# Performance work log

Measured on AMD Instinct MI355X. Metric: run time of the kernel, lower is better.

## Reference

```python
import jax, jax.numpy as jnp
import numpy as np

IGNORE_ID = -1
NEG_INF = -jnp.inf


def ctc_force_align(log_probs, ctc_label):
    """Viterbi forced alignment, vectorized over batch, scan over time.

    log_probs: [B, T, V] log-softmaxed CTC outputs (blank = 0).
    ctc_label: [B, L] int labels in [1, V).
    Returns align: [B, L] float32, begin frame (1-based, t+1) of each label.
    Assumes uniform lengths: input_len = T, target_len = L for every item
    (how the inputs are generated here).
    """
    B, T, V = log_probs.shape
    L = ctc_label.shape[1]
    N = 2 * L + 1  # CTC state lattice: blank,label,blank,...

    labels = jnp.zeros((B, N), dtype=ctc_label.dtype).at[:, 1::2].set(ctc_label)
    # per-state emission log-prob: [B, T, N]
    lab_b = jnp.broadcast_to(labels[:, None, :], (B, T, N))
    lp_states = jnp.take_along_axis(log_probs, lab_b, axis=2)

    idx = jnp.arange(N)
    ihalf = idx.astype(jnp.float32) / 2.0
    # labels[i] == labels[i-2] (False for i < 2)
    same_label = labels == jnp.concatenate(
        [jnp.full((B, 2), -1, labels.dtype), labels[:, :-2]], axis=1)
    two_way = (idx % 2 == 0)[None, :] | (idx == 1)[None, :] | same_label  # [B, N]

    ts = jnp.arange(T).astype(jnp.float32)
    # infeasible if i/2 > t or L - i/2 > T - t  (float division as in original)
    feas = ~((ihalf[None, :] > ts[:, None]) |
             (float(L) - ihalf[None, :] > float(T) - ts[:, None]))  # [T, N]

    a0 = jnp.where(idx[None, :] < 2, lp_states[:, 0, :], NEG_INF)  # [B, N]

    def shift(x, k):
        return jnp.pad(x, ((0, 0), (k, 0)), constant_values=NEG_INF)[:, :N]

    def step(a_prev, inputs):
        lp_t, feas_t = inputs  # [B, N], [N]
        p0, p1, p2 = a_prev, shift(a_prev, 1), shift(a_prev, 2)
        val_two = jnp.where(p0 > p1, idx, idx - 1)
        best0 = (p0 > p1) & (p0 > p2)
        best1 = (p1 > p0) & (p1 > p2)
        val_three = jnp.where(best0, idx, jnp.where(best1, idx - 1, idx - 2))
        val = jnp.where(idx[None, :] == 0, 0,
                        jnp.where(two_way, val_two, val_three))
        off = idx[None, :] - val
        a_sel = jnp.where(off == 0, p0, jnp.where(off == 1, p1, p2))
        a_new = jnp.where(feas_t[None, :], a_sel + lp_t, NEG_INF)
        v = jnp.where(feas_t[None, :], val, 0).astype(jnp.int32)
        return a_new, v

    lp_tb = jnp.moveaxis(lp_states, 1, 0)  # [T, B, N]
    a_final, v_all = jax.lax.scan(step, a0, (lp_tb[1:], feas[1:]))
    # v_all: [T-1, B, N] for t = 1 .. T-1
    v_all = jnp.moveaxis(v_all, 1, 0)  # [B, T-1, N]

    def backtrace(a_fin, v_seq):  # a_fin: [N], v_seq: [T-1, N]
        use_last = a_fin[N - 1] > a_fin[N - 2]
        pre0 = jnp.where(use_last, N - 1, N - 2)
        align0 = jnp.where((jnp.arange(L) == L - 1) & (~use_last),
                           float(T), 0.0).astype(jnp.float32)
        tp1 = jnp.arange(T - 1, 0, -1)  # t+1 values: T-1 .. 1
        lidx = jnp.arange(L)

        def bstep(carry, inp):
            pre, align = carry
            v_row, t1 = inp
            pre = v_row[pre]
            odd = (pre % 2) == 1
            align = jnp.where((lidx == pre // 2) & odd,
                              t1.astype(jnp.float32), align)
            return (pre, align), None

        (_, align), _ = jax.lax.scan(bstep, (pre0, align0), (v_seq[::-1], tp1))
        return align

    return jax.vmap(backtrace)(a_final, v_all)  # [B, L]


def setup_inputs() -> dict:
    key = jax.random.key(0)
    k0, k1, k2, k3, k4 = jax.random.split(key, 5)
    B, layers, L, T, V = 16, 6, 200, 1000, 5000
    ali_out = jax.random.uniform(k0, (B, layers, L + 1, T), dtype=jnp.float32)
    ali_beg = jax.random.randint(k1, (B, L), 0, T, dtype=jnp.int32)
    ali_end = jax.random.randint(k2, (B, L), 0, T, dtype=jnp.int32)
    enc_mask = jnp.zeros((B, T), dtype=bool)
    ctc_out = jax.random.normal(k3, (B, T, V), dtype=jnp.float32)
    ctc_label = jax.random.randint(k4, (B, L), 1, V, dtype=jnp.int32)
    ctc_len = jnp.full((B,), T, dtype=jnp.int32)
    return {"ali_out": ali_out, "ali_beg": ali_beg, "ali_end": ali_end,
            "enc_mask": enc_mask, "ctc_out": ctc_out,
            "ctc_label": ctc_label, "ctc_len": ctc_len}


def reference(ali_out, ali_beg, ali_end, enc_mask, ctc_out, ctc_label, ctc_len):
    B, layers, olen, ilen = ali_out.shape
    hlen = enc_mask.shape[1]  # == ilen == T
    # forced alignment on detached (stop-gradient) log-probs
    log_probs = jax.lax.stop_gradient(jax.nn.log_softmax(ctc_out, axis=2))
    ali = ctc_force_align(log_probs, ctc_label)  # [B, L] float32
    # expected position: matmul with pos_vec = [1..hlen], drop last output step
    pos = jnp.arange(1, hlen + 1, dtype=ali_out.dtype)
    ali_pos = jnp.einsum('bloi,i->blo', ali_out, pos)[:, :, :-1]  # [B, layers, L]
    ylens = jnp.sum(ali_beg != IGNORE_ID, axis=1)  # [B]
    mask = jnp.arange(olen - 1)[None, :] >= ylens[:, None]  # [B, L] pad mask
    total = (~mask).sum().astype(ali_out.dtype) * layers
    lat = jnp.where(mask[:, None, :], 0.0, ali_pos - ali[:, None, :])
    return (lat ** 2).sum() / total / hlen
```

## Files before the change

### kernel.cpp

```cpp
#include <hip/hip_runtime.h>
#include <hip/hip_bf16.h>
#include <math.h>

#define NEGINF (-INFINITY)

typedef float f32x4 __attribute__((ext_vector_type(4)));

__device__ __forceinline__ float wave_max_f(float m) {
#pragma unroll
  for (int d = 32; d > 0; d >>= 1) m = fmaxf(m, __shfl_xor(m, d, 64));
  return m;
}
__device__ __forceinline__ float wave_sum_f(float s) {
#pragma unroll
  for (int d = 32; d > 0; d >>= 1) s += __shfl_xor(s, d, 64);
  return s;
}
__device__ __forceinline__ int wave_sum_i(int s) {
#pragma unroll
  for (int d = 32; d > 0; d >>= 1) s += __shfl_xor(s, d, 64);
  return s;
}

__device__ __forceinline__ float dpp_wave_shr1(float x) {
  int r = __builtin_amdgcn_mov_dpp(__float_as_int(x), 0x138, 0xf, 0xf, true);
  return __int_as_float(r);
}

__global__ __launch_bounds__(256) void kA_lse_gather(
    const float* __restrict__ ctc_out, const int* __restrict__ ctc_label,
    float* __restrict__ lp, int B, int T, int V, int L, int LANES,
    int TPAD, int ROWF)
{
  extern __shared__ float shrow[];
  __shared__ float wred[4];
  int row = blockIdx.x;
  int b = row / T;
  int t = row - b * T;
  int tid = threadIdx.x;
  int w = tid >> 6;
  const float* x = ctc_out + (size_t)row * V;

  float m = NEGINF;
  int nf4 = V >> 2;
  for (int k = tid; k < nf4; k += 256) {
    float4 v = reinterpret_cast<const float4*>(x)[k];
    reinterpret_cast<float4*>(shrow)[k] = v;
    m = fmaxf(m, fmaxf(fmaxf(v.x, v.y), fmaxf(v.z, v.w)));
  }
  for (int k = (nf4 << 2) + tid; k < V; k += 256) {
    float v = x[k]; shrow[k] = v; m = fmaxf(m, v);
  }
  m = wave_max_f(m);
  if ((tid & 63) == 0) wred[w] = m;
  __syncthreads();
  float bm = fmaxf(fmaxf(wred[0], wred[1]), fmaxf(wred[2], wred[3]));
  __syncthreads();

  float s = 0.f;
  for (int k = tid; k < V; k += 256) s += __expf(shrow[k] - bm);
  s = wave_sum_f(s);
  if ((tid & 63) == 0) wred[w] = s;
  __syncthreads();
  float lse = bm + __logf(wred[0] + wred[1] + wred[2] + wred[3]);

  const int* lab = ctc_label + (size_t)b * L;
  float* dst = lp + ((size_t)b * TPAD + t) * ROWF;
  int nq = LANES * 4;
  for (int idx = tid; idx < nq; idx += 256) {
    int sl = idx >> 2, q = idx & 3;
    int jb = ((7 * sl) >> 1) + 1;
    int j = jb + q; if (j > L) j = L;
    int vi = lab[j - 1];
    if ((unsigned)vi >= (unsigned)V) vi = 0;
    dst[idx] = shrow[vi] - lse;
  }
  if (tid == 0) dst[nq] = shrow[0] - lse;
  for (int z = nq + 1 + tid; z < ROWF; z += 256) dst[z] = 0.f;
}

__global__ __launch_bounds__(64, 1) void kB_viterbi(
    const float* __restrict__ lp, const int* __restrict__ ctc_label,
    float* __restrict__ ali, int B, int T, int L, int TPAD, int ROWF)
{
  extern __shared__ float smemf[];
  const int N = 2 * L + 1;
  const int LANES = (N + 6) / 7;

  int b = blockIdx.x;
  int lane = threadIdx.x;
  const float* lpb = lp + (size_t)b * TPAD * ROWF;
  const int* lab = ctc_label + (size_t)b * L;
  int qlane = (lane < LANES) ? lane : LANES;
  int blkoff = LANES * 4;

  int i0 = lane * 7;
  float a0v, a1v, a2v, a3v, a4v, a5v, a6v;
  unsigned twmask = 0;
#pragma unroll
  for (int s = 0; s < 7; ++s) {
    int i = i0 + s;
    bool valid = (i < N);
    bool odd = (i & 1) != 0;
    int li = (i - 1) >> 1;
    int myl = (odd && valid) ? lab[li] : 0;
    int pl  = (odd && valid && i >= 3) ? lab[li - 1] : -1;
    if ((!odd) || (i == 1) || (myl == pl)) twmask |= (1u << s);
  }

  {
    f32x4 q00 = *reinterpret_cast<const f32x4*>(lpb + qlane * 4);
    float bl00 = lpb[blkoff];
    a0v = (i0 == 0) ? bl00 : NEGINF;
    a1v = NEGINF; a2v = NEGINF; a3v = NEGINF; a4v = NEGINF; a5v = NEGINF;
    a6v = NEGINF;
    if (i0 + 1 == 1) a1v = q00.x;
  }

  f32x4 rq0, rq1, rq2, rq3, rq4, rq5, rq6, rq7;
  unsigned short* offrow_w = (unsigned short*)smemf;

  asm volatile("s_waitcnt vmcnt(0) lgkmcnt(0)");
  __builtin_amdgcn_sched_barrier(0);

  unsigned long long base64 = (unsigned long long)lpb;
  unsigned voff = (unsigned)(qlane * 16) + 960u;

#define LOADQ(SL)                                                             \
  asm volatile("global_load_dwordx4 %0, %1, %2"                               \
               : "=v"(rq##SL) : "v"(voff), "s"(base64));                      \
  voff += 960u;

  LOADQ(1) LOADQ(2) LOADQ(3) LOADQ(4) LOADQ(5) LOADQ(6) LOADQ(7) LOADQ(0)

#define STEP_F(s, P0, P1, P2, OCS, ND, OD)                                    \
  {                                                                           \
    bool c01 = (P0) > (P1);                                                   \
    float m01 = c01 ? (P0) : (P1);                                            \
    bool allow3 = ((twmask >> (s)) & 1u) == 0u;                               \
    bool take3 = allow3 && !(m01 > (P2));                                     \
    float asel = take3 ? (P2) : m01;                                          \
    OD = take3 ? 2u : (c01 ? 0u : 1u);                                        \
    float lps = (((lane + (s)) & 1) ? (OCS) : blc);                           \
    ND = asel + lps;                                                          \
  }

#define STEP_S(s, P0, P1, P2, OCS, ND, OD)                                    \
  {                                                                           \
    STEP_F(s, P0, P1, P2, OCS, ND, OD)                                        \
    bool feas = ((s) >= lo_i) && ((s) <= hi_i);                               \
    ND = feas ? ND : NEGINF;                                                  \
  }

#define BODYC(SL, K, STEPM)                                                   \
  {                                                                           \
    const int tt = tt0 + (K);                                                 \
    int lo_i = 2 * (L - T + tt) - i0;                \
    int hi_i = 2 * tt - i0;                          \
    (void)lo_i; (void)hi_i;                                                   \
    asm volatile("s_waitcnt vmcnt(7)");                                       \
    __builtin_amdgcn_sched_barrier(0);                                        \
    float blc = __int_as_float(                                               \
        __builtin_amdgcn_readlane(__float_as_int(rq##SL.x), 58));             \
    float n0, n1, n2, n3, n4, n5, n6;                                         \
    unsigned o0, o1, o2, o3, o4, o5, o6;                                      \
    STEPM(5, a5v, a4v, a3v, rq##SL.z, n5, o5)                                 \
    STEPM(6, a6v, a5v, a4v, rq##SL.w, n6, o6)                                 \
    float t6n = dpp_wave_shr1(n6);                                            \
    float t5n = dpp_wave_shr1(n5);                                            \
    STEPM(0, a0v, t6, t5, rq##SL.x, n0, o0)                                   \
    STEPM(1, a1v, a0v, t6, rq##SL.x, n1, o1)                                  \
    STEPM(2, a2v, a1v, a0v, rq##SL.y, n2, o2)                                 \
    STEPM(3, a3v, a2v, a1v, rq##SL.y, n3, o3)                                 \
    STEPM(4, a4v, a3v, a2v, rq##SL.z, n4, o4)                                 \
    unsigned pack = o0 | (o1 << 2) | (o2 << 4) | (o3 << 6) | (o4 << 8) |      \
                    (o5 << 10) | (o6 << 12);                                  \
    offrow_w[(size_t)(tt - 1) * 64 + lane] = (unsigned short)pack;            \
    LOADQ(SL)                                                                 \
    a0v = n0; a1v = n1; a2v = n2; a3v = n3; a4v = n4; a5v = n5; a6v = n6;     \
    t6 = (lane == 0) ? NEGINF : t6n;                                          \
    t5 = (lane == 0) ? NEGINF : t5n;                                          \
  }

  float t6 = __shfl_up(a6v, 1, 64);
  float t5 = __shfl_up(a5v, 1, 64);
  if (lane == 0) { t6 = NEGINF; t5 = NEGINF; }

  int tt0 = 1;
  for (; tt0 + 8 <= T; tt0 += 8) {
    if (tt0 >= L && tt0 + 7 <= T - L) {
      BODYC(1, 0, STEP_F) BODYC(2, 1, STEP_F) BODYC(3, 2, STEP_F)
      BODYC(4, 3, STEP_F) BODYC(5, 4, STEP_F) BODYC(6, 5, STEP_F)
      BODYC(7, 6, STEP_F) BODYC(0, 7, STEP_F)
    } else {
      BODYC(1, 0, STEP_S) BODYC(2, 1, STEP_S) BODYC(3, 2, STEP_S)
      BODYC(4, 3, STEP_S) BODYC(5, 4, STEP_S) BODYC(6, 5, STEP_S)
      BODYC(7, 6, STEP_S) BODYC(0, 7, STEP_S)
    }
  }
  {
    int rem = T - tt0;
    if (rem > 0) { BODYC(1, 0, STEP_S) }
    if (rem > 1) { BODYC(2, 1, STEP_S) }
    if (rem > 2) { BODYC(3, 2, STEP_S) }
    if (rem > 3) { BODYC(4, 3, STEP_S) }
    if (rem > 4) { BODYC(5, 4, STEP_S) }
    if (rem > 5) { BODYC(6, 5, STEP_S) }
    if (rem > 6) { BODYC(7, 6, STEP_S) }
  }
#undef BODYC
#undef STEP_S
#undef STEP_F
#undef LOADQ

  asm volatile("s_waitcnt vmcnt(0) lgkmcnt(0)" ::: "memory");
  __builtin_amdgcn_sched_barrier(0);
  asm volatile("" :: "v"(rq0), "v"(rq1), "v"(rq2), "v"(rq3));
  asm volatile("" :: "v"(rq4), "v"(rq5), "v"(rq6), "v"(rq7));

  int iN1 = N - 1, iN2 = N - 2;
  auto pick = [&](int sIdx) {
    float r = a0v;
    r = (sIdx == 1) ? a1v : r;
    r = (sIdx == 2) ? a2v : r;
    r = (sIdx == 3) ? a3v : r;
    r = (sIdx == 4) ? a4v : r;
    r = (sIdx == 5) ? a5v : r;
    r = (sIdx == 6) ? a6v : r;
    return r;
  };
  float vlast = __shfl(pick(iN1 % 7), iN1 / 7, 64);
  float vprev = __shfl(pick(iN2 % 7), iN2 / 7, 64);
  bool use_last = vlast > vprev;
  int pre = use_last ? iN1 : iN2;

  float al[4] = {0.f, 0.f, 0.f, 0.f};
  {
    int lbl = L - 1; int rr = lbl >> 6, ln = lbl & 63;
#pragma unroll
    for (int r = 0; r < 4; ++r)
      if (!use_last && rr == r && lane == ln) al[r] = (float)T;
  }

  const unsigned short* offrow = (const unsigned short*)smemf;
  int t = T - 1;
  int g = pre / 7, mm = pre - g * 7;
  while (t >= 1) {
    int K = (t < 7) ? t : 7;
    int pcur = g * 7 + mm;
    int gmax = g;
    unsigned short w0v = offrow[(size_t)(t - 1) * 64 + g];
    unsigned short cw[7][3];
    int gmn[7];
#pragma unroll
    for (int j = 1; j < 7; ++j) {
      if (j < K) {
        int lo = pcur - 2 * j; if (lo < 0) lo = 0;
        int gm = lo / 7;
        gmn[j] = gm;
#pragma unroll
        for (int r = 0; r < 3; ++r) {
          int gg = gm + r; if (gg > gmax) gg = gmax;
          cw[j][r] = offrow[(size_t)(t - 1 - j) * 64 + gg];
        }
      }
    }
#pragma unroll
    for (int j = 0; j < 7; ++j) {
      if (j < K) {
        unsigned w;
        if (j == 0) {
          w = w0v;
        } else {
          int gi = g - gmn[j];
          unsigned wva = cw[j][0], wvb = cw[j][1], wvc = cw[j][2];
          w = (gi == 0) ? wva : ((gi == 1) ? wvb : wvc);
        }
        unsigned off = (w >> (2 * mm)) & 3u;
        mm -= (int)off;
        bool bor = mm < 0;
        g = bor ? (g - 1) : g;
        mm = bor ? (mm + 7) : mm;
        int cur = g * 7 + mm;
        if (cur & 1) {
          int lbl = cur >> 1;
          int rr = lbl >> 6, ln = lbl & 63;
#pragma unroll
          for (int r = 0; r < 4; ++r)
            if (rr == r && lane == ln) al[r] = (float)(t - j);
        }
      }
    }
    t -= K;
  }

#pragma unroll
  for (int r = 0; r < 4; ++r) {
    int l = lane + 64 * r;
    if (l < L) ali[(size_t)b * L + l] = al[r];
  }
}

__global__ __launch_bounds__(256) void kC_rows(
    const float* __restrict__ ali_out, const float* __restrict__ ali,
    const int* __restrict__ ali_beg, float* __restrict__ partials,
    int B, int layers, int L, int T)
{
  __shared__ float ps[4];
  int wid = threadIdx.x >> 6, lane = threadIdx.x & 63;
  int row = blockIdx.x * 4 + wid;
  int nrows = B * layers * L;
  float val = 0.f;
  if (row < nrows) {
    int o = row % L;
    int bl = row / L;
    int layer = bl % layers;
    int b = bl / layers;
    const float* x = ali_out + ((size_t)(b * layers + layer) * (L + 1) + o) * T;
    float s = 0.f;
    if ((T & 3) == 0) {
      int nf4 = T >> 2;
      for (int k = lane; k < nf4; k += 64) {
        float4 v = reinterpret_cast<const float4*>(x)[k];
        float base = (float)(4 * k);
        s += v.x * (base + 1.f) + v.y * (base + 2.f) +
             v.z * (base + 3.f) + v.w * (base + 4.f);
      }
    } else {
      for (int k = lane; k < T; k += 64) s += x[k] * (float)(k + 1);
    }
    s = wave_sum_f(s);
    int cnt = 0;
    for (int l = lane; l < L; l += 64)
      cnt += (ali_beg[(size_t)b * L + l] != -1) ? 1 : 0;
    cnt = wave_sum_i(cnt);
    if (lane == 0) {
      float lat = (o >= cnt) ? 0.f : (s - ali[(size_t)b * L + o]);
      val = lat * lat;
    }
  }
  if (lane == 0) ps[wid] = val;
  __syncthreads();
  if (threadIdx.x == 0) partials[blockIdx.x] = ps[0] + ps[1] + ps[2] + ps[3];
}

__global__ __launch_bounds__(256) void kD_final(
    const float* __restrict__ partials, int nparts,
    const int* __restrict__ ali_beg, int BL, int layers, int T,
    float* __restrict__ out)
{
  __shared__ float wred[4];
  __shared__ int wcnt[4];
  int tid = threadIdx.x, w = tid >> 6;
  float s = 0.f;
  for (int k = tid; k < nparts; k += 256) s += partials[k];
  s = wave_sum_f(s);
  int c = 0;
  for (int k = tid; k < BL; k += 256) c += (ali_beg[k] != -1) ? 1 : 0;
  c = wave_sum_i(c);
  if ((tid & 63) == 0) { wred[w] = s; wcnt[w] = c; }
  __syncthreads();
  if (tid == 0) {
    float ss = wred[0] + wred[1] + wred[2] + wred[3];
    float total = (float)(wcnt[0] + wcnt[1] + wcnt[2] + wcnt[3]) * (float)layers;
    out[0] = ss / total / (float)T;
  }
}

extern "C" void kernel_launch(void* const* d_in, const int* in_sizes, int n_in,
                              void* d_out, int out_size, void* d_ws, size_t ws_size,
                              hipStream_t stream)
{
  const float* ali_out   = (const float*)d_in[0];
  const int*   ali_beg   = (const int*)d_in[1];
  const float* ctc_out   = (const float*)d_in[4];
  const int*   ctc_label = (const int*)d_in[5];

  int B = in_sizes[6];
  int L = in_sizes[1] / B;
  int T = in_sizes[3] / B;
  int V = (int)((long long)in_sizes[4] / ((long long)B * T));
  int layers = (int)((long long)in_sizes[0] / ((long long)B * (L + 1) * T));

  int N = 2 * L + 1;
  int LANES = (N + 6) / 7;
  int ROWF = LANES * 4 + 8;
  int TPAD = T + 64;

  float* lp = (float*)d_ws;
  float* ali = lp + (size_t)B * TPAD * ROWF;
  float* partials = ali + (size_t)B * L;
  int nrows = B * layers * L;
  int gridC = (nrows + 3) / 4;

  size_t shA = (size_t)V * sizeof(float);
  hipLaunchKernelGGL(kA_lse_gather, dim3(B * T), dim3(256), shA, stream,
                     ctc_out, ctc_label, lp, B, T, V, L, LANES, TPAD, ROWF);

  size_t shB = (size_t)(T - 1) * 128;
  hipFuncSetAttribute(reinterpret_cast<const void*>(kB_viterbi),
                      hipFuncAttributeMaxDynamicSharedMemorySize, (int)shB);
  hipLaunchKernelGGL(kB_viterbi, dim3(B), dim3(64), shB, stream,
                     lp, ctc_label, ali, B, T, L, TPAD, ROWF);

  hipLaunchKernelGGL(kC_rows, dim3(gridC), dim3(256), 0, stream,
                     ali_out, ali, ali_beg, partials, B, layers, L, T);

  hipLaunchKernelGGL(kD_final, dim3(1), dim3(256), 0, stream,
                     partials, gridC, ali_beg, B * L, layers, T, (float*)d_out);
}
```

Baseline: 476.1 us.

## Stage Viterbi emissions into LDS ring via producer waves

The Viterbi kernel grows from one wave to four. Waves 1 and 2 act as producers that copy 16-timestep segments of the emission table into a triple-buffered LDS ring, and wave 0 reads each step with ds_read instead of global loads. The goal is to take global memory latency off the serial recurrence and replace it with shorter LDS latency. The backpointer table is packed to a 58-entry stride, down from 64. In exchange, a __syncthreads is added per segment, and it hardcodes the segment size (15360 bytes per stage, row 960 bytes) for the specific L.

```diff
diff --git a/kernel.cpp b/kernel.cpp
--- a/kernel.cpp
+++ b/kernel.cpp
@@ -79,20 +79,47 @@
   for (int z = nq + 1 + tid; z < ROWF; z += 256) dst[z] = 0.f;
 }
 
-__global__ __launch_bounds__(64, 1) void kB_viterbi(
+__global__ __launch_bounds__(256, 1) void kB_viterbi(
     const float* __restrict__ lp, const int* __restrict__ ctc_label,
     float* __restrict__ ali, int B, int T, int L, int TPAD, int ROWF)
 {
   extern __shared__ float smemf[];
   const int N = 2 * L + 1;
   const int LANES = (N + 6) / 7;
+  const unsigned STGB = 15360u;
+  const unsigned OFFBASE = 3u * STGB;
 
   int b = blockIdx.x;
-  int lane = threadIdx.x;
+  int tid = threadIdx.x;
+  int wid = tid >> 6;
+  int lane = tid & 63;
   const float* lpb = lp + (size_t)b * TPAD * ROWF;
+  int NSEG = (T - 1 + 15) >> 4;
+
+  auto stage_seg = [&](int k) {
+    const f32x4* src =
+        reinterpret_cast<const f32x4*>(lpb + (size_t)(1 + 16 * k) * ROWF);
+    f32x4* dst = reinterpret_cast<f32x4*>(
+        reinterpret_cast<char*>(smemf) + (unsigned)(k % 3) * STGB);
+#pragma unroll
+    for (int kk = 0; kk < 15; ++kk) dst[kk * 64 + lane] = src[kk * 64 + lane];
+  };
+
+  if (wid != 0) {
+    if (wid == 1 && NSEG > 0) stage_seg(0);
+    if (wid == 2 && NSEG > 1) stage_seg(1);
+    __syncthreads();
+    for (int sg = 0; sg < NSEG; ++sg) {
+      int k = sg + 2;
+      if (k < NSEG && wid == 1 + (k & 1)) stage_seg(k);
+      __syncthreads();
+    }
+    return;
+  }
+
   const int* lab = ctc_label + (size_t)b * L;
   int qlane = (lane < LANES) ? lane : LANES;
-  int blkoff = LANES * 4;
+  unsigned qoff = (unsigned)(qlane * 16);
 
   int i0 = lane * 7;
   float a0v, a1v, a2v, a3v, a4v, a5v, a6v;
@@ -110,30 +137,38 @@
 
   {
     f32x4 q00 = *reinterpret_cast<const f32x4*>(lpb + qlane * 4);
-    float bl00 = lpb[blkoff];
+    float bl00 = lpb[LANES * 4];
     a0v = (i0 == 0) ? bl00 : NEGINF;
     a1v = NEGINF; a2v = NEGINF; a3v = NEGINF; a4v = NEGINF; a5v = NEGINF;
     a6v = NEGINF;
     if (i0 + 1 == 1) a1v = q00.x;
   }
-
-  f32x4 rq0, rq1, rq2, rq3, rq4, rq5, rq6, rq7;
-  unsigned short* offrow_w = (unsigned short*)smemf;
-
-  asm volatile("s_waitcnt vmcnt(0) lgkmcnt(0)");
-  __builtin_amdgcn_sched_barrier(0);
-
-  unsigned long long base64 = (unsigned long long)lpb;
-  unsigned voff = (unsigned)(qlane * 16) + 960u;
-
-#define LOADQ(SL)                                                             \
-  asm volatile("global_load_dwordx4 %0, %1, %2"                               \
-               : "=v"(rq##SL) : "v"(voff), "s"(base64));                      \
-  voff += 960u;
-
-  LOADQ(1) LOADQ(2) LOADQ(3) LOADQ(4) LOADQ(5) LOADQ(6) LOADQ(7) LOADQ(0)
-
-#define STEP_F(s, P0, P1, P2, OCS, ND, OD)                                    \
+  float t6 = __shfl_up(a6v, 1, 64);
+  float t5 = __shfl_up(a5v, 1, 64);
+  if (lane == 0) { t6 = NEGINF; t5 = NEGINF; }
+
+  __syncthreads();
+
+  f32x4 rqA, rqB, rqC, rqD;
+  float rblA, rblB, rblC, rblD;
+
+#define RINGRD(SL, qaddr, baddr)                                              \
+  asm volatile("ds_read_b128 %0, %1" : "=v"(rq##SL) : "v"(qaddr));            \
+  asm volatile("ds_read_b32 %0, %1" : "=v"(rbl##SL) : "v"(baddr));
+
+  unsigned wa = OFFBASE + (unsigned)(lane * 2);
+  {
+    RINGRD(A, 0u * 960u + qoff, 0u * 960u + 928u)
+    RINGRD(B, 1u * 960u + qoff, 1u * 960u + 928u)
+    RINGRD(C, 2u * 960u + qoff, 2u * 960u + 928u)
+    RINGRD(D, 3u * 960u + qoff, 3u * 960u + 928u)
+    unsigned zz = 0;
+    asm volatile("ds_write_b16 %0, %1" :: "v"(wa), "v"(zz));
+    asm volatile("ds_write_b16 %0, %1" :: "v"(wa), "v"(zz));
+    asm volatile("ds_write_b16 %0, %1" :: "v"(wa), "v"(zz));
+  }
+
+#define STEPX(s, P0, P1, P2, OCS, ND, OD)                                     \
   {                                                                           \
     bool c01 = (P0) > (P1);                                                   \
     float m01 = c01 ? (P0) : (P1);                                            \
@@ -143,80 +178,87 @@
     OD = take3 ? 2u : (c01 ? 0u : 1u);                                        \
     float lps = (((lane + (s)) & 1) ? (OCS) : blc);                           \
     ND = asel + lps;                                                          \
-  }
-
-#define STEP_S(s, P0, P1, P2, OCS, ND, OD)                                    \
-  {                                                                           \
-    STEP_F(s, P0, P1, P2, OCS, ND, OD)                                        \
     bool feas = ((s) >= lo_i) && ((s) <= hi_i);                               \
     ND = feas ? ND : NEGINF;                                                  \
   }
 
-#define BODYC(SL, K, STEPM)                                                   \
+#define BODYX(SL, UL, WCNT, CLAMP)                                            \
   {                                                                           \
-    const int tt = tt0 + (K);                                                 \
-    int lo_i = 2 * (L - T + tt) - i0;                \
-    int hi_i = 2 * tt - i0;                          \
-    (void)lo_i; (void)hi_i;                                                   \
-    asm volatile("s_waitcnt vmcnt(7)");                                       \
+    const int tt = tt0 + (UL);                                                \
+    int lo_i = 2 * (L - T + tt) - i0;                                         \
+    int hi_i = 2 * tt - i0;                                                   \
+    asm volatile("s_waitcnt lgkmcnt(" #WCNT ")");                             \
     __builtin_amdgcn_sched_barrier(0);                                        \
-    float blc = __int_as_float(                                               \
-        __builtin_amdgcn_readlane(__float_as_int(rq##SL.x), 58));             \
+    float blc = rbl##SL;                                                      \
+    f32x4 oc = rq##SL;                                                        \
     float n0, n1, n2, n3, n4, n5, n6;                                         \
     unsigned o0, o1, o2, o3, o4, o5, o6;                                      \
-    STEPM(5, a5v, a4v, a3v, rq##SL.z, n5, o5)                                 \
-    STEPM(6, a6v, a5v, a4v, rq##SL.w, n6, o6)                                 \
+    STEPX(5, a5v, a4v, a3v, oc.z, n5, o5)                                     \
+    STEPX(6, a6v, a5v, a4v, oc.w, n6, o6)                                     \
     float t6n = dpp_wave_shr1(n6);                                            \
     float t5n = dpp_wave_shr1(n5);                                            \
-    STEPM(0, a0v, t6, t5, rq##SL.x, n0, o0)                                   \
-    STEPM(1, a1v, a0v, t6, rq##SL.x, n1, o1)                                  \
-    STEPM(2, a2v, a1v, a0v, rq##SL.y, n2, o2)                                 \
-    STEPM(3, a3v, a2v, a1v, rq##SL.y, n3, o3)                                 \
-    STEPM(4, a4v, a3v, a2v, rq##SL.z, n4, o4)                                 \
+    STEPX(0, a0v, t6, t5, oc.x, n0, o0)                                       \
+    STEPX(1, a1v, a0v, t6, oc.x, n1, o1)                                      \
+    STEPX(2, a2v, a1v, a0v, oc.y, n2, o2)                                     \
+    STEPX(3, a3v, a2v, a1v, oc.y, n3, o3)                                     \
+    STEPX(4, a4v, a3v, a2v, oc.z, n4, o4)                                     \
     unsigned pack = o0 | (o1 << 2) | (o2 << 4) | (o3 << 6) | (o4 << 8) |      \
                     (o5 << 10) | (o6 << 12);                                  \
-    offrow_w[(size_t)(tt - 1) * 64 + lane] = (unsigned short)pack;            \
-    LOADQ(SL)                                                                 \
+    if (lane < LANES)                                                         \
+      asm volatile("ds_write_b16 %0, %1" :: "v"(wa), "v"(pack));              \
+    wa += 116;                                                                \
+    {                                                                         \
+      unsigned rbase;                                                         \
+      if (CLAMP) {                                                            \
+        rbase = bufc + (((UL) < 12) ? ((UL) + 4) : 15) * 960u;                \
+      } else {                                                                \
+        rbase = ((UL) < 12) ? (bufc + ((UL) + 4) * 960u)                      \
+                            : (bufn + ((UL) - 12) * 960u);                    \
+      }                                                                       \
+      RINGRD(SL, rbase + qoff, rbase + 928u)                                  \
+    }                                                                         \
     a0v = n0; a1v = n1; a2v = n2; a3v = n3; a4v = n4; a5v = n5; a6v = n6;     \
     t6 = (lane == 0) ? NEGINF : t6n;                                          \
     t5 = (lane == 0) ? NEGINF : t5n;                                          \
   }
 
-  float t6 = __shfl_up(a6v, 1, 64);
-  float t5 = __shfl_up(a5v, 1, 64);
-  if (lane == 0) { t6 = NEGINF; t5 = NEGINF; }
-
-  int tt0 = 1;
-  for (; tt0 + 8 <= T; tt0 += 8) {
-    if (tt0 >= L && tt0 + 7 <= T - L) {
-      BODYC(1, 0, STEP_F) BODYC(2, 1, STEP_F) BODYC(3, 2, STEP_F)
-      BODYC(4, 3, STEP_F) BODYC(5, 4, STEP_F) BODYC(6, 5, STEP_F)
-      BODYC(7, 6, STEP_F) BODYC(0, 7, STEP_F)
+  for (int sg = 0; sg < NSEG; ++sg) {
+    int tt0 = 1 + 16 * sg;
+    unsigned bufc = (unsigned)(sg % 3) * STGB;
+    unsigned bufn = (sg + 1 < NSEG) ? (unsigned)((sg + 1) % 3) * STGB : bufc;
+    int rem = T - tt0;
+    if (rem >= 16) {
+      BODYX(A, 0, 9, 0)  BODYX(B, 1, 9, 0)  BODYX(C, 2, 9, 0)
+      BODYX(D, 3, 9, 0)  BODYX(A, 4, 9, 0)  BODYX(B, 5, 9, 0)
+      BODYX(C, 6, 9, 0)  BODYX(D, 7, 9, 0)  BODYX(A, 8, 9, 0)
+      BODYX(B, 9, 9, 0)  BODYX(C, 10, 9, 0) BODYX(D, 11, 9, 0)
+      BODYX(A, 12, 9, 0) BODYX(B, 13, 9, 0) BODYX(C, 14, 9, 0)
+      BODYX(D, 15, 9, 0)
     } else {
-      BODYC(1, 0, STEP_S) BODYC(2, 1, STEP_S) BODYC(3, 2, STEP_S)
-      BODYC(4, 3, STEP_S) BODYC(5, 4, STEP_S) BODYC(6, 5, STEP_S)
-      BODYC(7, 6, STEP_S) BODYC(0, 7, STEP_S)
-    }
-  }
-  {
-    int rem = T - tt0;
-    if (rem > 0) { BODYC(1, 0, STEP_S) }
-    if (rem > 1) { BODYC(2, 1, STEP_S) }
-    if (rem > 2) { BODYC(3, 2, STEP_S) }
-    if (rem > 3) { BODYC(4, 3, STEP_S) }
-    if (rem > 4) { BODYC(5, 4, STEP_S) }
-    if (rem > 5) { BODYC(6, 5, STEP_S) }
-    if (rem > 6) { BODYC(7, 6, STEP_S) }
-  }
-#undef BODYC
-#undef STEP_S
-#undef STEP_F
-#undef LOADQ
+      if (rem > 0)  { BODYX(A, 0, 0, 1) }
+      if (rem > 1)  { BODYX(B, 1, 0, 1) }
+      if (rem > 2)  { BODYX(C, 2, 0, 1) }
+      if (rem > 3)  { BODYX(D, 3, 0, 1) }
+      if (rem > 4)  { BODYX(A, 4, 0, 1) }
+      if (rem > 5)  { BODYX(B, 5, 0, 1) }
+      if (rem > 6)  { BODYX(C, 6, 0, 1) }
+      if (rem > 7)  { BODYX(D, 7, 0, 1) }
+      if (rem > 8)  { BODYX(A, 8, 0, 1) }
+      if (rem > 9)  { BODYX(B, 9, 0, 1) }
+      if (rem > 10) { BODYX(C, 10, 0, 1) }
+      if (rem > 11) { BODYX(D, 11, 0, 1) }
+      if (rem > 12) { BODYX(A, 12, 0, 1) }
+      if (rem > 13) { BODYX(B, 13, 0, 1) }
+      if (rem > 14) { BODYX(C, 14, 0, 1) }
+    }
+    __syncthreads();
+  }
+#undef BODYX
+#undef STEPX
+#undef RINGRD
 
   asm volatile("s_waitcnt vmcnt(0) lgkmcnt(0)" ::: "memory");
   __builtin_amdgcn_sched_barrier(0);
-  asm volatile("" :: "v"(rq0), "v"(rq1), "v"(rq2), "v"(rq3));
-  asm volatile("" :: "v"(rq4), "v"(rq5), "v"(rq6), "v"(rq7));
 
   int iN1 = N - 1, iN2 = N - 2;
   auto pick = [&](int sIdx) {
@@ -242,14 +284,15 @@
       if (!use_last && rr == r && lane == ln) al[r] = (float)T;
   }
 
-  const unsigned short* offrow = (const unsigned short*)smemf;
+  const unsigned short* offrow =
+      (const unsigned short*)((char*)smemf + OFFBASE);
   int t = T - 1;
   int g = pre / 7, mm = pre - g * 7;
   while (t >= 1) {
     int K = (t < 7) ? t : 7;
     int pcur = g * 7 + mm;
     int gmax = g;
-    unsigned short w0v = offrow[(size_t)(t - 1) * 64 + g];
+    unsigned short w0v = offrow[(size_t)(t - 1) * 58 + g];
     unsigned short cw[7][3];
     int gmn[7];
 #pragma unroll
@@ -261,7 +304,7 @@
 #pragma unroll
         for (int r = 0; r < 3; ++r) {
           int gg = gm + r; if (gg > gmax) gg = gmax;
-          cw[j][r] = offrow[(size_t)(t - 1 - j) * 64 + gg];
+          cw[j][r] = offrow[(size_t)(t - 1 - j) * 58 + gg];
         }
       }
     }
@@ -397,10 +440,10 @@
   hipLaunchKernelGGL(kA_lse_gather, dim3(B * T), dim3(256), shA, stream,
                      ctc_out, ctc_label, lp, B, T, V, L, LANES, TPAD, ROWF);
 
-  size_t shB = (size_t)(T - 1) * 128;
+  size_t shB = (size_t)3 * 15360 + (size_t)(T - 1) * 116;
   hipFuncSetAttribute(reinterpret_cast<const void*>(kB_viterbi),
                       hipFuncAttributeMaxDynamicSharedMemorySize, (int)shB);
-  hipLaunchKernelGGL(kB_viterbi, dim3(B), dim3(64), shB, stream,
+  hipLaunchKernelGGL(kB_viterbi, dim3(B), dim3(256), shB, stream,
                      lp, ctc_label, ali, B, T, L, TPAD, ROWF);
 
   hipLaunchKernelGGL(kC_rows, dim3(gridC), dim3(256), 0, stream,
```

Measured after the change: 565.9 us. 18.9% more time.
